# Kernel optimization log

Measured on AMD Instinct MI355X. Metric: run time of the kernel, lower is better.

Reference implementation:

```python
import jax, jax.numpy as jnp
import numpy as np

IMAGE_SIZE = 1024
DOWNSIZING = 64
THRESHOLD = 0.65  # default_threshold_target (threshold arg == 0)
NUM_BG_POINTS = 1
ORI_SHAPE = (2160, 3840)
EMBED_C, FEAT_H, FEAT_W = 256, 64, 64


def setup_inputs() -> dict:
    key = jax.random.key(0)
    k1, k2 = jax.random.split(key)
    image_embeddings = jax.random.normal(k1, (1, EMBED_C, FEAT_H, FEAT_W), dtype=jnp.float32)
    reference_feat = jax.random.normal(k2, (1, EMBED_C), dtype=jnp.float32) * 0.1
    ori_shape = jnp.array(ORI_SHAPE, dtype=jnp.int32)
    return {"image_embeddings": image_embeddings, "reference_feat": reference_feat, "ori_shape": ori_shape}


def _postprocess_masks(sim, H, W):
    # F.interpolate to (image_size, image_size), crop to pre-padded size, resize to ori_shape
    sim = jax.image.resize(sim, (1, 1, IMAGE_SIZE, IMAGE_SIZE), method="bilinear", antialias=False)
    scale = IMAGE_SIZE / max(H, W)
    ph = int(np.floor(H * scale + 0.5))
    pw = int(np.floor(W * scale + 0.5))
    sim = sim[..., :ph, :pw]
    return jax.image.resize(sim, (1, 1, H, W), method="bilinear", antialias=False)


def reference(image_embeddings, reference_feat, ori_shape):
    H, W = int(ori_shape[0]), int(ori_shape[1])
    # --- similarity map ---
    t = image_embeddings[0]                                   # (C, hf, wf)
    c, hf, wf = t.shape
    t = t / jnp.linalg.norm(t, axis=0, keepdims=True)         # channel-wise L2 norm
    sim = (reference_feat @ t.reshape(c, hf * wf)).reshape(1, 1, hf, wf)
    sim = _postprocess_masks(sim, H, W)
    m = sim[0, 0]                                             # (H, W)
    flat = m.reshape(-1)                                      # (H*W,)
    hw = H * W

    # --- background points: k smallest values ---
    _, bg_idx = jax.lax.top_k(-flat, NUM_BG_POINTS)
    bg_row = bg_idx // W
    bg_col = bg_idx % W
    bg_coords = jnp.stack([bg_col, bg_row], axis=1).astype(jnp.float32)  # (N, 2) = (x, y)

    # --- foreground points: grid-binned per-cell max (segment-max form of
    #     torch.where + unique + broadcast-equality + per-bin topk) ---
    ratio = IMAGE_SIZE / max(H, W)
    n_cells_side = IMAGE_SIZE // DOWNSIZING                    # 16; bounds grid rows/cols
    num_cells = n_cells_side * n_cells_side                    # 256 fixed
    idx = jnp.arange(hw, dtype=jnp.int32)
    ys = idx // W
    xs = idx % W
    gy = jnp.floor(ys * (ratio / DOWNSIZING)).astype(jnp.int32)
    gx = jnp.floor(xs * (ratio / DOWNSIZING)).astype(jnp.int32)
    seg = gy * n_cells_side + gx                               # grid id per pixel

    valid = flat > THRESHOLD
    masked = jnp.where(valid, flat, -jnp.inf)
    seg_max = jax.ops.segment_max(masked, seg, num_segments=num_cells)
    # first pixel achieving the cell max (matches torch.topk tie behavior)
    is_max = valid & (masked == seg_max[seg])
    cand = jnp.where(is_max, idx, hw)
    best = jax.ops.segment_min(cand, seg, num_segments=num_cells)
    cell_valid = best < hw
    bi = jnp.minimum(best, hw - 1)
    px = (bi % W).astype(jnp.float32)
    py = (bi // W).astype(jnp.float32)
    ps = flat[bi]
    points = jnp.stack([px, py, ps], axis=1)                   # (num_cells, 3) = (x, y, score)
    points = jnp.where(cell_valid[:, None], points, -1.0)      # mimic F.pad(value=-1) rows
    sort_key = jnp.where(cell_valid, ps, -jnp.inf)
    order = jnp.argsort(-sort_key)                             # score descending, invalid last
    points_scores = points[order]
    return points_scores, bg_coords
```

## Files before the change

kernel.cpp:

```cpp
#include <hip/hip_runtime.h>

#define W_OUT 3840
#define H_OUT 2160
#define IW 1024
#define IH 576

__device__ __forceinline__ unsigned int enc_f32(float f) {
    unsigned int b = __float_as_uint(f);
    return b ^ (0x80000000u | (unsigned int)((int)b >> 31));
}

__global__ __launch_bounds__(256) void sim_kernel(
    const float* __restrict__ emb, const float* __restrict__ ref,
    float* __restrict__ sim)
{
    const int lane = threadIdx.x & 63;
    const int wave = threadIdx.x >> 6;
    const int p = blockIdx.x * 64 + lane;
    const int cbase = wave * 64;
    float dot = 0.f, ss = 0.f;
#pragma unroll 8
    for (int cc = 0; cc < 64; ++cc) {
        int c = cbase + cc;
        float a = emb[c * 4096 + p];
        dot = fmaf(ref[c], a, dot);
        ss  = fmaf(a, a, ss);
    }
    __shared__ float sdot[4][64];
    __shared__ float sss[4][64];
    sdot[wave][lane] = dot;
    sss[wave][lane]  = ss;
    __syncthreads();
    if (wave == 0) {
        float d = (sdot[0][lane] + sdot[1][lane]) + (sdot[2][lane] + sdot[3][lane]);
        float s = (sss[0][lane] + sss[1][lane]) + (sss[2][lane] + sss[3][lane]);
        sim[p] = d / sqrtf(s);
    }
}

__global__ __launch_bounds__(256) void scan_kernel(
    const float* __restrict__ sim,
    unsigned long long* __restrict__ cellPart,
    unsigned long long* __restrict__ bgPart)
{
    __shared__ float4 I4[2][IW / 4];
    __shared__ unsigned long long wmin[4];
    float* I0 = (float*)&I4[0][0];
    float* I1 = (float*)&I4[1][0];

    const float INV375 = (float)(1.0 / 3.75);
    const float INV16  = 0.0625f;

    const int y   = blockIdx.x;
    const int tid = threadIdx.x;

    float fy  = ((float)y + 0.5f) * INV375 - 0.5f;
    float fyf = floorf(fy);
    float wy  = fy - fyf;
    int ai = (int)fyf;
    int a1 = min(max(ai + 1, 0), IH - 1);
    int a0 = min(max(ai,     0), IH - 1);

    for (int r = 0; r < 2; ++r) {
        int a = (r == 0) ? a0 : a1;
        float fa  = ((float)a + 0.5f) * INV16 - 0.5f;
        float faf = floorf(fa);
        float wa  = fa - faf;
        int si = (int)faf;
        int s1 = min(max(si + 1, 0), 63);
        int s0 = min(max(si,     0), 63);
        const float* row0 = sim + s0 * 64;
        const float* row1 = sim + s1 * 64;
        float* dst = (r == 0) ? I0 : I1;
        for (int b = tid; b < IW; b += 256) {
            float fb  = ((float)b + 0.5f) * INV16 - 0.5f;
            float fbf = floorf(fb);
            float wb  = fb - fbf;
            int ci = (int)fbf;
            int c1 = min(max(ci + 1, 0), 63);
            int c0 = min(max(ci,     0), 63);
            float v0 = row0[c0] * (1.f - wb) + row0[c1] * wb;
            float v1 = row1[c0] * (1.f - wb) + row1[c1] * wb;
            dst[b] = v0 * (1.f - wa) + v1 * wa;
        }
    }
    __syncthreads();

    unsigned long long bestCell = 0ull;
    unsigned long long bestBg   = 0xFFFFFFFFFFFFFFFFull;
    const int x0 = tid * 15;
    const unsigned int idxBase = (unsigned int)(y * W_OUT + x0);

#define UPD(F, jj) {                                                        \
        unsigned long long top = ((unsigned long long)enc_f32(F)) << 32;    \
        unsigned int idx = idxBase + (jj);                                  \
        unsigned long long bgk = top | (unsigned long long)idx;             \
        unsigned long long ck  = top | (unsigned long long)(~idx);          \
        if (ck  > bestCell) bestCell = ck;                                  \
        if (bgk < bestBg)   bestBg   = bgk;                                 \
    }

    if (tid == 0 || tid == 255) {
#pragma unroll
        for (int j = 0; j < 15; ++j) {
            int x = x0 + j;
            float fx  = ((float)x + 0.5f) * INV375 - 0.5f;
            float fxf = floorf(fx);
            float wx  = fx - fxf;
            int bi = (int)fxf;
            int b1 = min(max(bi + 1, 0), IW - 1);
            int b0 = min(max(bi,     0), IW - 1);
            float v0 = I0[b0] * (1.f - wx) + I0[b1] * wx;
            float v1 = I1[b0] * (1.f - wx) + I1[b1] * wx;
            float F  = v0 * (1.f - wy) + v1 * wy;
            UPD(F, j)
        }
    } else {
        float4 A0 = I4[0][tid - 1], B0 = I4[0][tid], C0 = I4[0][tid + 1];
        float4 A1 = I4[1][tid - 1], B1 = I4[1][tid], C1 = I4[1][tid + 1];
        const float rr0[12] = {A0.x,A0.y,A0.z,A0.w, B0.x,B0.y,B0.z,B0.w, C0.x,C0.y,C0.z,C0.w};
        const float rr1[12] = {A1.x,A1.y,A1.z,A1.w, B1.x,B1.y,B1.z,B1.w, C1.x,C1.y,C1.z,C1.w};

#define PX(j, i0) {                                                         \
            float fx  = ((float)(x0 + (j)) + 0.5f) * INV375 - 0.5f;         \
            float fxf = floorf(fx);                                         \
            float wx  = fx - fxf;                                           \
            float v0 = rr0[(i0)] * (1.f - wx) + rr0[(i0) + 1] * wx;         \
            float v1 = rr1[(i0)] * (1.f - wx) + rr1[(i0) + 1] * wx;         \
            float F  = v0 * (1.f - wy) + v1 * wy;                           \
            UPD(F, j)                                                       \
        }
        PX(0,3)  PX(1,3)  PX(2,4)  PX(3,4)  PX(4,4)
        PX(5,4)  PX(6,5)  PX(7,5)  PX(8,5)  PX(9,6)
        PX(10,6) PX(11,6) PX(12,6) PX(13,7) PX(14,7)
#undef PX
    }
#undef UPD

#pragma unroll
    for (int m = 1; m <= 8; m <<= 1) {
        unsigned long long o = __shfl_xor(bestCell, m, 64);
        if (o > bestCell) bestCell = o;
    }
    if ((tid & 15) == 0) cellPart[y * 16 + (tid >> 4)] = bestCell;

#pragma unroll
    for (int m = 1; m <= 32; m <<= 1) {
        unsigned long long o = __shfl_xor(bestBg, m, 64);
        if (o < bestBg) bestBg = o;
    }
    if ((tid & 63) == 0) wmin[tid >> 6] = bestBg;
    __syncthreads();
    if (tid == 0) {
        unsigned long long b0 = wmin[0] < wmin[1] ? wmin[0] : wmin[1];
        unsigned long long b1 = wmin[2] < wmin[3] ? wmin[2] : wmin[3];
        bgPart[y] = b0 < b1 ? b0 : b1;
    }
}

__global__ __launch_bounds__(256) void finalize_kernel(
    const unsigned long long* __restrict__ cellPart,
    const unsigned long long* __restrict__ bgPart,
    float* __restrict__ out)
{
    __shared__ float sk[256];
    __shared__ unsigned long long sb[256];
    const int t = threadIdx.x;

    unsigned long long best = 0ull;
    if (t < 144) {
        const int band = t >> 4, cx = t & 15;
        const unsigned long long* p = cellPart + (band * 240) * 16 + cx;
#pragma unroll 8
        for (int r = 0; r < 240; ++r) {
            unsigned long long k = p[r * 16];
            if (k > best) best = k;
        }
    }
    float px = -1.f, py = -1.f, ps = -1.f;
    float key = -__builtin_huge_valf();
    if (best != 0ull) {
        unsigned int e = (unsigned int)(best >> 32);
        unsigned int b = (e & 0x80000000u) ? (e ^ 0x80000000u) : ~e;
        float v = __uint_as_float(b);
        if (v > 0.65f) {
            unsigned int idx = ~((unsigned int)(best & 0xFFFFFFFFull));
            px = (float)(idx % W_OUT);
            py = (float)(idx / W_OUT);
            ps = v;
            key = v;
        }
    }

    unsigned long long m = 0xFFFFFFFFFFFFFFFFull;
    for (int i = t; i < H_OUT; i += 256) {
        unsigned long long k = bgPart[i];
        if (k < m) m = k;
    }
    sb[t] = m;
    __syncthreads();
    for (int s = 128; s > 0; s >>= 1) {
        if (t < s) {
            unsigned long long o = sb[t + s];
            if (o < sb[t]) sb[t] = o;
        }
        __syncthreads();
    }

    sk[t] = key;
    __syncthreads();
    int rank = 0;
    for (int j = 0; j < 256; ++j) {
        float kj = sk[j];
        if (kj > key || (kj == key && j < t)) rank++;
    }
    out[rank * 3 + 0] = px;
    out[rank * 3 + 1] = py;
    out[rank * 3 + 2] = ps;
    if (t == 0) {
        unsigned int idx = (unsigned int)(sb[0] & 0xFFFFFFFFull);
        out[256 * 3 + 0] = (float)(idx % W_OUT);
        out[256 * 3 + 1] = (float)(idx / W_OUT);
    }
}

extern "C" void kernel_launch(void* const* d_in, const int* in_sizes, int n_in,
                              void* d_out, int out_size, void* d_ws, size_t ws_size,
                              hipStream_t stream) {
    (void)in_sizes; (void)n_in; (void)out_size; (void)ws_size;
    const float* emb = (const float*)d_in[0];
    const float* ref = (const float*)d_in[1];
    float* out = (float*)d_out;

    float* sim = (float*)d_ws;
    unsigned long long* cellPart = (unsigned long long*)((char*)d_ws + 16384);
    unsigned long long* bgPart   = cellPart + H_OUT * 16;

    sim_kernel<<<64, 256, 0, stream>>>(emb, ref, sim);
    scan_kernel<<<H_OUT, 256, 0, stream>>>(sim, cellPart, bgPart);
    finalize_kernel<<<1, 256, 0, stream>>>(cellPart, bgPart, out);
}
```

Baseline: 99.62 us.

## Precompute intermediate 1024-wide resize rows in separate kernel and parallelize finalize reduction

Adds an inter_kernel that computes the 576x1024 intermediate bilinear image once, instead of each of the 2160 scan blocks rebuilding two rows in shared memory. The scan kernel now reads its two source rows straight from global memory, with no LDS staging and no block barrier. Each scan block writes per-wave background minima, which drops the second shared-memory reduction. Finalize now uses all threads to pre-reduce the cell partials into LDS before the per-cell max, replacing a 240-step serial loop per thread. The cost is an extra kernel launch and a roughly 2.3 MB workspace buffer whose rows are re-read from cache.

```diff
diff --git a/kernel.cpp b/kernel.cpp
--- a/kernel.cpp
+++ b/kernel.cpp
@@ -38,19 +38,46 @@
     }
 }
 
+__global__ __launch_bounds__(256) void inter_kernel(
+    const float* __restrict__ sim, float* __restrict__ I)
+{
+    const int a   = blockIdx.x;
+    const int tid = threadIdx.x;
+    const float INV16 = 0.0625f;
+
+    float fa  = ((float)a + 0.5f) * INV16 - 0.5f;
+    float faf = floorf(fa);
+    float wa  = fa - faf;
+    int si = (int)faf;
+    int s1 = min(max(si + 1, 0), 63);
+    int s0 = min(max(si,     0), 63);
+    const float* row0 = sim + s0 * 64;
+    const float* row1 = sim + s1 * 64;
+
+    float4 o;
+    float* po = &o.x;
+#pragma unroll
+    for (int k = 0; k < 4; ++k) {
+        int b = tid * 4 + k;
+        float fb  = ((float)b + 0.5f) * INV16 - 0.5f;
+        float fbf = floorf(fb);
+        float wb  = fb - fbf;
+        int ci = (int)fbf;
+        int c1 = min(max(ci + 1, 0), 63);
+        int c0 = min(max(ci,     0), 63);
+        float v0 = row0[c0] * (1.f - wb) + row0[c1] * wb;
+        float v1 = row1[c0] * (1.f - wb) + row1[c1] * wb;
+        po[k] = v0 * (1.f - wa) + v1 * wa;
+    }
+    *(float4*)(I + a * IW + tid * 4) = o;
+}
+
 __global__ __launch_bounds__(256) void scan_kernel(
-    const float* __restrict__ sim,
+    const float* __restrict__ I,
     unsigned long long* __restrict__ cellPart,
     unsigned long long* __restrict__ bgPart)
 {
-    __shared__ float4 I4[2][IW / 4];
-    __shared__ unsigned long long wmin[4];
-    float* I0 = (float*)&I4[0][0];
-    float* I1 = (float*)&I4[1][0];
-
     const float INV375 = (float)(1.0 / 3.75);
-    const float INV16  = 0.0625f;
-
     const int y   = blockIdx.x;
     const int tid = threadIdx.x;
 
@@ -60,31 +87,8 @@
     int ai = (int)fyf;
     int a1 = min(max(ai + 1, 0), IH - 1);
     int a0 = min(max(ai,     0), IH - 1);
-
-    for (int r = 0; r < 2; ++r) {
-        int a = (r == 0) ? a0 : a1;
-        float fa  = ((float)a + 0.5f) * INV16 - 0.5f;
-        float faf = floorf(fa);
-        float wa  = fa - faf;
-        int si = (int)faf;
-        int s1 = min(max(si + 1, 0), 63);
-        int s0 = min(max(si,     0), 63);
-        const float* row0 = sim + s0 * 64;
-        const float* row1 = sim + s1 * 64;
-        float* dst = (r == 0) ? I0 : I1;
-        for (int b = tid; b < IW; b += 256) {
-            float fb  = ((float)b + 0.5f) * INV16 - 0.5f;
-            float fbf = floorf(fb);
-            float wb  = fb - fbf;
-            int ci = (int)fbf;
-            int c1 = min(max(ci + 1, 0), 63);
-            int c0 = min(max(ci,     0), 63);
-            float v0 = row0[c0] * (1.f - wb) + row0[c1] * wb;
-            float v1 = row1[c0] * (1.f - wb) + row1[c1] * wb;
-            dst[b] = v0 * (1.f - wa) + v1 * wa;
-        }
-    }
-    __syncthreads();
+    const float* R0 = I + a0 * IW;
+    const float* R1 = I + a1 * IW;
 
     unsigned long long bestCell = 0ull;
     unsigned long long bestBg   = 0xFFFFFFFFFFFFFFFFull;
@@ -110,29 +114,31 @@
             int bi = (int)fxf;
             int b1 = min(max(bi + 1, 0), IW - 1);
             int b0 = min(max(bi,     0), IW - 1);
-            float v0 = I0[b0] * (1.f - wx) + I0[b1] * wx;
-            float v1 = I1[b0] * (1.f - wx) + I1[b1] * wx;
+            float v0 = R0[b0] * (1.f - wx) + R0[b1] * wx;
+            float v1 = R1[b0] * (1.f - wx) + R1[b1] * wx;
             float F  = v0 * (1.f - wy) + v1 * wy;
             UPD(F, j)
         }
     } else {
-        float4 A0 = I4[0][tid - 1], B0 = I4[0][tid], C0 = I4[0][tid + 1];
-        float4 A1 = I4[1][tid - 1], B1 = I4[1][tid], C1 = I4[1][tid + 1];
-        const float rr0[12] = {A0.x,A0.y,A0.z,A0.w, B0.x,B0.y,B0.z,B0.w, C0.x,C0.y,C0.z,C0.w};
-        const float rr1[12] = {A1.x,A1.y,A1.z,A1.w, B1.x,B1.y,B1.z,B1.w, C1.x,C1.y,C1.z,C1.w};
+        const float* b0p = R0 + 4 * tid;
+        const float* b1p = R1 + 4 * tid;
+        float4 B0 = *(const float4*)b0p;
+        float4 B1 = *(const float4*)b1p;
+        const float f0[6] = {b0p[-1], B0.x, B0.y, B0.z, B0.w, b0p[4]};
+        const float f1[6] = {b1p[-1], B1.x, B1.y, B1.z, B1.w, b1p[4]};
 
 #define PX(j, i0) {                                                         \
             float fx  = ((float)(x0 + (j)) + 0.5f) * INV375 - 0.5f;         \
             float fxf = floorf(fx);                                         \
             float wx  = fx - fxf;                                           \
-            float v0 = rr0[(i0)] * (1.f - wx) + rr0[(i0) + 1] * wx;         \
-            float v1 = rr1[(i0)] * (1.f - wx) + rr1[(i0) + 1] * wx;         \
+            float v0 = f0[(i0)] * (1.f - wx) + f0[(i0) + 1] * wx;           \
+            float v1 = f1[(i0)] * (1.f - wx) + f1[(i0) + 1] * wx;           \
             float F  = v0 * (1.f - wy) + v1 * wy;                           \
             UPD(F, j)                                                       \
         }
-        PX(0,3)  PX(1,3)  PX(2,4)  PX(3,4)  PX(4,4)
-        PX(5,4)  PX(6,5)  PX(7,5)  PX(8,5)  PX(9,6)
-        PX(10,6) PX(11,6) PX(12,6) PX(13,7) PX(14,7)
+        PX(0,0)  PX(1,0)  PX(2,1)  PX(3,1)  PX(4,1)
+        PX(5,1)  PX(6,2)  PX(7,2)  PX(8,2)  PX(9,3)
+        PX(10,3) PX(11,3) PX(12,3) PX(13,4) PX(14,4)
 #undef PX
     }
 #undef UPD
@@ -149,13 +155,7 @@
         unsigned long long o = __shfl_xor(bestBg, m, 64);
         if (o < bestBg) bestBg = o;
     }
-    if ((tid & 63) == 0) wmin[tid >> 6] = bestBg;
-    __syncthreads();
-    if (tid == 0) {
-        unsigned long long b0 = wmin[0] < wmin[1] ? wmin[0] : wmin[1];
-        unsigned long long b1 = wmin[2] < wmin[3] ? wmin[2] : wmin[3];
-        bgPart[y] = b0 < b1 ? b0 : b1;
-    }
+    if ((tid & 63) == 0) bgPart[y * 4 + (tid >> 6)] = bestBg;
 }
 
 __global__ __launch_bounds__(256) void finalize_kernel(
@@ -163,18 +163,38 @@
     const unsigned long long* __restrict__ bgPart,
     float* __restrict__ out)
 {
+    __shared__ unsigned long long sB[9 * 256];
     __shared__ float sk[256];
     __shared__ unsigned long long sb[256];
     const int t = threadIdx.x;
 
+#pragma unroll
+    for (int band = 0; band < 9; ++band) {
+        unsigned long long acc = 0ull;
+        const unsigned long long* p = cellPart + band * 3840 + t;
+#pragma unroll
+        for (int j = 0; j < 15; ++j) {
+            unsigned long long k = p[j * 256];
+            if (k > acc) acc = k;
+        }
+        sB[band * 256 + t] = acc;
+    }
+
+    unsigned long long m = 0xFFFFFFFFFFFFFFFFull;
+    for (int i = t; i < H_OUT * 4; i += 256) {
+        unsigned long long k = bgPart[i];
+        if (k < m) m = k;
+    }
+    sb[t] = m;
+    __syncthreads();
+
     unsigned long long best = 0ull;
     if (t < 144) {
-        const int band = t >> 4, cx = t & 15;
-        const unsigned long long* p = cellPart + (band * 240) * 16 + cx;
-#pragma unroll 8
-        for (int r = 0; r < 240; ++r) {
-            unsigned long long k = p[r * 16];
-            if (k > best) best = k;
+        int band = t >> 4, cx = t & 15;
+#pragma unroll
+        for (int k = 0; k < 16; ++k) {
+            unsigned long long v = sB[band * 256 + k * 16 + cx];
+            if (v > best) best = v;
         }
     }
     float px = -1.f, py = -1.f, ps = -1.f;
@@ -192,13 +212,6 @@
         }
     }
 
-    unsigned long long m = 0xFFFFFFFFFFFFFFFFull;
-    for (int i = t; i < H_OUT; i += 256) {
-        unsigned long long k = bgPart[i];
-        if (k < m) m = k;
-    }
-    sb[t] = m;
-    __syncthreads();
     for (int s = 128; s > 0; s >>= 1) {
         if (t < s) {
             unsigned long long o = sb[t + s];
@@ -233,10 +246,12 @@
     float* out = (float*)d_out;
 
     float* sim = (float*)d_ws;
-    unsigned long long* cellPart = (unsigned long long*)((char*)d_ws + 16384);
+    float* I   = (float*)((char*)d_ws + 16384);
+    unsigned long long* cellPart = (unsigned long long*)((char*)d_ws + 16384 + IH * IW * 4);
     unsigned long long* bgPart   = cellPart + H_OUT * 16;
 
     sim_kernel<<<64, 256, 0, stream>>>(emb, ref, sim);
-    scan_kernel<<<H_OUT, 256, 0, stream>>>(sim, cellPart, bgPart);
+    inter_kernel<<<IH, 256, 0, stream>>>(sim, I);
+    scan_kernel<<<H_OUT, 256, 0, stream>>>(I, cellPart, bgPart);
     finalize_kernel<<<1, 256, 0, stream>>>(cellPart, bgPart, out);
 }
```

After: 100.8 us. About the same (+1.2%).
